# Optimization experiments

Measured on AMD Instinct MI355X. Metric: run time of the kernel, lower is better.

Reference implementation:

```python
import jax, jax.numpy as jnp
import numpy as np

ALPHA = 0.2
TOP_K = 32

def setup_inputs() -> dict:
    key = jax.random.key(0)
    k1, k2, k3, k4, k5 = jax.random.split(key, 5)
    B, T, N, D = 2, 12, 8192, 256
    X = jax.random.normal(k1, (B, T, N, D), dtype=jnp.float32)
    E1 = jax.random.normal(k2, (N, D), dtype=jnp.float32)
    E2 = jax.random.normal(k3, (N, D), dtype=jnp.float32)
    theta1 = jax.random.normal(k4, (D, D), dtype=jnp.float32)
    theta2 = jax.random.normal(k5, (D, D), dtype=jnp.float32)
    a = jnp.float32(1.0)
    return {"X": X, "E1": E1, "E2": E2, "theta1": theta1, "theta2": theta2, "a": a}

def reference(X, E1, E2, theta1, theta2, a):
    # X: [B, T, N, D]
    N = X.shape[2]
    X0 = X.mean(axis=1)[0]  # [N, D], mean over time, first batch element
    # Row-wise L2 normalize (F.normalize with eps=1e-12)
    norm = jnp.maximum(jnp.linalg.norm(X0, axis=1, keepdims=True), 1e-12)
    X_norm = X0 / norm
    sim = X_norm @ X_norm.T  # [N, N] cosine similarity
    sim = sim * (1.0 - jnp.eye(N, dtype=sim.dtype))  # zero diagonal
    topk_vals, topk_idx = jax.lax.top_k(sim, TOP_K)  # [N, K]
    rows = jnp.arange(N)[:, None]
    A_base = jnp.zeros_like(sim).at[rows, topk_idx].set(topk_vals)
    # Adaptive dependency matrix
    M1 = jnp.tanh(ALPHA * (E1 @ theta1))  # [N, D]
    M2 = jnp.tanh(ALPHA * (E2 @ theta2))  # [N, D]
    diff = M1 @ M2.T - M2 @ M1.T  # [N, N], antisymmetric
    adaptive = jax.nn.relu(jnp.tanh(a * diff))
    return adaptive * A_base
```

## Files before the change

kernel.cpp:

```cpp
#include <hip/hip_runtime.h>
#include <hip/hip_bf16.h>
#include <hip/hip_fp16.h>
#include <float.h>
#include <math.h>

#define NN 8192
#define DD 256
#define TT 12
#define TOPK 32
#define NQ 4
#define CAP 56
#define UCAP 64
#define TAU0 0.146875f
#define B2 2.2e-3f
#define DIFFCUT 3.0f

typedef __attribute__((ext_vector_type(8))) _Float16 f16x8;
typedef __attribute__((ext_vector_type(16))) float f32x16;
typedef __attribute__((ext_vector_type(4))) float f32x4;

__device__ __forceinline__ unsigned short f2h(float x) {
    __half h = __float2half(x);
    return *(unsigned short*)&h;
}
__device__ __forceinline__ float h2f(unsigned short v) {
    __half h = *(__half*)&v;
    return __half2float(h);
}

__global__ __launch_bounds__(256) void k_mean_norm(const float* __restrict__ X,
                                                   float* __restrict__ Xn,
                                                   unsigned short* __restrict__ Xpk) {
    const int row = blockIdx.x;
    const int d = threadIdx.x;
    const float* base = X + (size_t)row * DD + d;
    double s = 0.0;
#pragma unroll
    for (int t = 0; t < TT; ++t) s += (double)base[(size_t)t * NN * DD];
    const double mean = s / 12.0;

    double ss = mean * mean;
#pragma unroll
    for (int o = 32; o > 0; o >>= 1) ss += __shfl_down(ss, o, 64);
    __shared__ double wss[4];
    const int lane = threadIdx.x & 63, w = threadIdx.x >> 6;
    if (lane == 0) wss[w] = ss;
    __syncthreads();
    double nrm = sqrt(wss[0] + wss[1] + wss[2] + wss[3]);
    if (nrm < 1e-12) nrm = 1e-12;
    const float xv = (float)(mean / nrm);
    Xn[(size_t)row * DD + d] = xv;

    const int cb = row >> 5;
    const int ks = d >> 4;
    const int l = (row & 31) + 32 * ((d >> 3) & 1);
    const int e = d & 7;
    Xpk[(((size_t)cb * 16 + ks) * 64 + l) * 8 + e] = f2h(xv);
}

__global__ __launch_bounds__(256, 3) void k_simcand_M(
    const unsigned short* __restrict__ Xpk,
    const float* __restrict__ E1, const float* __restrict__ E2,
    const float* __restrict__ th1, const float* __restrict__ th2,
    float* __restrict__ M1, float* __restrict__ M2,
    unsigned int* __restrict__ Mpk,
    unsigned short* __restrict__ cand, float* __restrict__ candv,
    int* __restrict__ counts, float* __restrict__ out) {
    __shared__ __align__(16) unsigned char smem[27264];

    const int tid = threadIdx.x;
    const int g = blockIdx.x;

    if (g < 1280) {
        const int slot = g % 5;
        if (slot == 4) {
            const int zid = g / 5;
            const f32x4 zz = {0.f, 0.f, 0.f, 0.f};
            f32x4* zp = (f32x4*)out + (size_t)zid * 65536 + tid;
#pragma unroll 8
            for (int i = 0; i < 256; ++i)
                __builtin_nontemporal_store(zz, zp + i * 256);
            return;
        }
        unsigned short* a_lds = (unsigned short*)smem;
        int* cnt = (int*)(smem + 16384);
        unsigned short* lst = (unsigned short*)(smem + 16512);
        float* lstv = (float*)(smem + 20096);

        const int simIdx = (g / 5) * 4 + slot;
        const int nt = tid >> 6, lane = tid & 63;
        const int bx = simIdx & 255;
        const int quarter = simIdx >> 8;
        const int r0 = bx * 32;

        {
            const f32x4* src = (const f32x4*)(Xpk + (size_t)bx * 8192);
            f32x4* dst = (f32x4*)a_lds;
            for (int i = tid; i < 1024; i += 256) dst[i] = src[i];
        }
        for (int i = tid; i < 32; i += 256) cnt[i] = 0;
        __syncthreads();

        const int rowL = (lane >> 5) << 2;
        const int colL = lane & 31;
        const unsigned short* arow = a_lds + lane * 8;

        for (int c = 0; c < 16; ++c) {
            const int cbB = quarter * 64 + c * 4 + nt;
            const int gcol = cbB * 32 + colL;
            const size_t bbase = ((size_t)cbB * 16) * 512 + lane * 8;

            f16x8 b[16];
#pragma unroll
            for (int ks = 0; ks < 16; ++ks)
                b[ks] = *(const f16x8*)(Xpk + bbase + ks * 512);

            f32x16 acc;
#pragma unroll
            for (int q = 0; q < 16; ++q) acc[q] = 0.f;
#pragma unroll
            for (int ks = 0; ks < 16; ++ks)
                acc = __builtin_amdgcn_mfma_f32_32x32x16_f16(
                    *(const f16x8*)(arow + ks * 512), b[ks], acc, 0, 0, 0);

#pragma unroll
            for (int reg = 0; reg < 16; ++reg) {
                const float v = acc[reg];
                if (v > TAU0) {
                    const int rl = rowL + (reg & 3) + ((reg >> 2) << 3);
                    if (r0 + rl != gcol) {
                        const int idx = atomicAdd(&cnt[rl], 1);
                        if (idx < CAP) {
                            lst[rl * CAP + idx] = (unsigned short)gcol;
                            lstv[rl * CAP + idx] = v;
                        }
                    }
                }
            }
        }
        __syncthreads();
        for (int i = tid; i < 32; i += 256) {
            int n = cnt[i];
            counts[(r0 + i) * NQ + quarter] = n > CAP ? CAP : n;
        }
        for (int i = tid; i < 32 * CAP; i += 256) {
            const int rl = i / CAP, k = i % CAP;
            int n = cnt[rl];
            if (n > CAP) n = CAP;
            if (k < n) {
                const size_t o = ((size_t)(r0 + rl) * NQ + quarter) * CAP + k;
                cand[o] = lst[rl * CAP + k];
                candv[o] = lstv[rl * CAP + k];
            }
        }
    } else {
        float* e1 = (float*)smem;
        float* e2 = (float*)(smem + 8192);
        const int r0 = (g - 1280) * 8;
        {
            const f32x4* E14 = (const f32x4*)(E1 + (size_t)r0 * DD);
            const f32x4* E24 = (const f32x4*)(E2 + (size_t)r0 * DD);
            f32x4* e14 = (f32x4*)e1;
            f32x4* e24 = (f32x4*)e2;
            for (int i = tid; i < 512; i += 256) {
                e14[i] = E14[i];
                e24[i] = E24[i];
            }
        }
        __syncthreads();
        const int j = tid;
        float a1[8], a2[8];
#pragma unroll
        for (int r = 0; r < 8; ++r) { a1[r] = 0.f; a2[r] = 0.f; }
        for (int k = 0; k < DD; k += 4) {
            float t1[4], t2[4];
#pragma unroll
            for (int kk = 0; kk < 4; ++kk) {
                t1[kk] = th1[(size_t)(k + kk) * DD + j];
                t2[kk] = th2[(size_t)(k + kk) * DD + j];
            }
#pragma unroll
            for (int r = 0; r < 8; ++r) {
                const f32x4 ev1 = *(const f32x4*)&e1[r * DD + k];
                const f32x4 ev2 = *(const f32x4*)&e2[r * DD + k];
                a1[r] += ev1.x * t1[0];
                a1[r] += ev1.y * t1[1];
                a1[r] += ev1.z * t1[2];
                a1[r] += ev1.w * t1[3];
                a2[r] += ev2.x * t2[0];
                a2[r] += ev2.y * t2[1];
                a2[r] += ev2.z * t2[2];
                a2[r] += ev2.w * t2[3];
            }
        }
#pragma unroll
        for (int r = 0; r < 8; ++r) {
            const float m1v = tanhf(0.2f * a1[r]);
            const float m2v = tanhf(0.2f * a2[r]);
            M1[(size_t)(r0 + r) * DD + j] = m1v;
            M2[(size_t)(r0 + r) * DD + j] = m2v;
            Mpk[(size_t)(r0 + r) * DD + j] =
                ((unsigned)f2h(m2v) << 16) | (unsigned)f2h(m1v);
        }
    }
}

__global__ __launch_bounds__(256) void k_refine(
    const float* __restrict__ Xn, const unsigned short* __restrict__ cand,
    const float* __restrict__ candv, const int* __restrict__ counts,
    const float* __restrict__ M1, const float* __restrict__ M2,
    const unsigned int* __restrict__ Mpk, const float* __restrict__ a_ptr,
    float* __restrict__ out) {
    __shared__ float xi[DD], m1i[DD], m2i[DD];
    __shared__ unsigned short cidx[NQ * CAP];
    __shared__ float cs[NQ * CAP];
    __shared__ int carr[NQ], offs[NQ + 1];
    __shared__ unsigned short uidx[UCAP];
    __shared__ float ue[UCAP];
    __shared__ int nUs, ms;
    __shared__ float wv[TOPK];
    __shared__ int wj[TOPK];

    const int i = blockIdx.x, t = threadIdx.x;

    xi[t]  = Xn[(size_t)i * DD + t];
    m1i[t] = M1[(size_t)i * DD + t];
    m2i[t] = M2[(size_t)i * DD + t];
    if (t < NQ) {
        int n = counts[i * NQ + t];
        carr[t] = n < 0 ? 0 : (n > CAP ? CAP : n);
    }
    if (t < TOPK) { wv[t] = 0.f; wj[t] = i; }
    if (t == 0) { nUs = 0; ms = 0; }
    __syncthreads();
    if (t == 0) {
        int s = 0;
#pragma unroll
        for (int q = 0; q < NQ; ++q) { offs[q] = s; s += carr[q]; }
        offs[NQ] = s;
    }
    __syncthreads();
    const int nc = offs[NQ];
#pragma unroll
    for (int q = 0; q < NQ; ++q)
        if (t < carr[q]) {
            const size_t o = ((size_t)i * NQ + q) * CAP + t;
            cidx[offs[q] + t] = cand[o];
            cs[offs[q] + t] = candv[o];
        }
    __syncthreads();

    if (t < nc) {
        const float vc = cs[t];
        int possAbove = 0, certAbove = 0;
        for (int k = 0; k < nc; ++k) {
            const float vk = cs[k];
            possAbove += (vk >= vc - B2);
            certAbove += (vk > vc + B2);
        }
        possAbove -= 1;
        if (possAbove <= TOPK - 1) {
            const int slot = atomicAdd(&ms, 1);
            wv[slot] = vc;
            wj[slot] = cidx[t];
        } else if (certAbove < TOPK) {
            const int p = atomicAdd(&nUs, 1);
            if (p < UCAP) uidx[p] = cidx[t];
        }
    }
    __syncthreads();
    const int m = ms;
    int nU = nUs;
    if (nU > UCAP) nU = UCAP;

    if (nU > 0) {
        const int dl = t & 15, cg = t >> 4;
        for (int base = 0; base < nU; base += 16) {
            const int c = base + cg;
            float p = 0.f;
            if (c < nU) {
                const int j = uidx[c];
                const f32x4* xj4 = (const f32x4*)(Xn + (size_t)j * DD) + dl * 4;
                const f32x4* xi4 = (const f32x4*)xi + dl * 4;
#pragma unroll
                for (int q = 0; q < 4; ++q) {
                    const f32x4 A = xi4[q], B = xj4[q];
                    p += A.x * B.x;
                    p += A.y * B.y;
                    p += A.z * B.z;
                    p += A.w * B.w;
                }
            }
#pragma unroll
            for (int o = 1; o < 16; o <<= 1) p += __shfl_xor(p, o, 64);
            if (c < nU && dl == 0) ue[c] = p;
        }
        __syncthreads();
        if (t < nU && m < TOPK) {
            const float vc = ue[t];
            const int jc = uidx[t];
            int r = 0;
            for (int k = 0; k < nU; ++k) {
                const float vk = ue[k];
                r += (vk > vc) || (vk == vc && uidx[k] < jc);
            }
            if (r < TOPK - m) {
                wv[m + r] = vc;
                wj[m + r] = jc;
            }
        }
        __syncthreads();
    }

    const float a = *a_ptr;
    const int g = t >> 3, lg = t & 7;
    const int j = wj[g];
    const float v = wv[g];

    float p1 = 0.f;
    {
        const uint4* mp = (const uint4*)(Mpk + (size_t)j * DD) + lg * 8;
#pragma unroll
        for (int q = 0; q < 8; ++q) {
            const uint4 u = mp[q];
            const int d = lg * 32 + q * 4;
            p1 += m1i[d + 0] * h2f((unsigned short)(u.x >> 16)) -
                  m2i[d + 0] * h2f((unsigned short)(u.x & 0xffff));
            p1 += m1i[d + 1] * h2f((unsigned short)(u.y >> 16)) -
                  m2i[d + 1] * h2f((unsigned short)(u.y & 0xffff));
            p1 += m1i[d + 2] * h2f((unsigned short)(u.z >> 16)) -
                  m2i[d + 2] * h2f((unsigned short)(u.z & 0xffff));
            p1 += m1i[d + 3] * h2f((unsigned short)(u.w >> 16)) -
                  m2i[d + 3] * h2f((unsigned short)(u.w & 0xffff));
        }
    }
#pragma unroll
    for (int o = 4; o > 0; o >>= 1) p1 += __shfl_xor(p1, o, 64);

    float diff = p1;
    if (fabsf(diff) < DIFFCUT) {
        const f32x4* m1j4 = (const f32x4*)(M1 + (size_t)j * DD) + lg * 8;
        const f32x4* m2j4 = (const f32x4*)(M2 + (size_t)j * DD) + lg * 8;
        float p = 0.f;
        const int dbase = lg * 32;
#pragma unroll
        for (int q = 0; q < 8; ++q) {
            const f32x4 b1 = m1j4[q], b2 = m2j4[q];
            const int d = dbase + q * 4;
            p += m1i[d + 0] * b2.x - m2i[d + 0] * b1.x;
            p += m1i[d + 1] * b2.y - m2i[d + 1] * b1.y;
            p += m1i[d + 2] * b2.z - m2i[d + 2] * b1.z;
            p += m1i[d + 3] * b2.w - m2i[d + 3] * b1.w;
        }
#pragma unroll
        for (int o = 4; o > 0; o >>= 1) p += __shfl_xor(p, o, 64);
        diff = p;
    }
    if (lg == 0 && j != i) {
        float ad = tanhf(a * diff);
        ad = ad > 0.f ? ad : 0.f;
        out[(size_t)i * NN + j] = ad * v;
    }
}

extern "C" void kernel_launch(void* const* d_in, const int* in_sizes, int n_in,
                              void* d_out, int out_size, void* d_ws, size_t ws_size,
                              hipStream_t stream) {
    const float* X   = (const float*)d_in[0];
    const float* E1  = (const float*)d_in[1];
    const float* E2  = (const float*)d_in[2];
    const float* th1 = (const float*)d_in[3];
    const float* th2 = (const float*)d_in[4];
    const float* a   = (const float*)d_in[5];
    float* out = (float*)d_out;

    float* ws = (float*)d_ws;
    float* Xn = ws;
    float* M1 = Xn + (size_t)NN * DD;
    float* M2 = M1 + (size_t)NN * DD;
    unsigned short* Xpk = (unsigned short*)(M2 + (size_t)NN * DD);
    unsigned int* Mpk = (unsigned int*)(Xpk + (size_t)NN * DD);
    unsigned short* cand = (unsigned short*)(Mpk + (size_t)NN * DD);
    float* candv = (float*)(cand + (size_t)NN * NQ * CAP);
    int* counts = (int*)(candv + (size_t)NN * NQ * CAP);

    k_mean_norm<<<NN, 256, 0, stream>>>(X, Xn, Xpk);
    k_simcand_M<<<2304, 256, 0, stream>>>(Xpk, E1, E2, th1, th2,
                                          M1, M2, Mpk,
                                          cand, candv, counts, out);
    k_refine<<<NN, 256, 0, stream>>>(Xn, cand, candv, counts, M1, M2, Mpk, a, out);
}
```

Baseline: 252.4 us.

## Retile similarity GEMM to 64-row blocks with double-buffered LDS staging, move zeroing to refine

The similarity/candidate kernel now computes 64x256 output tiles per block, four waves in a 2x2 arrangement, with 4 accumulators each. A and B fragments are staged into LDS through global_load_lds with double buffering over the K steps, replacing per-wave direct global loads of B. A 32-row A tile is no longer held whole in LDS. The output zeroing blocks are removed from this kernel. Instead each refine block zeroes its own output row before scattering. This cuts redundant global traffic and raises MFMA reuse, at the cost of higher LDS use, lower occupancy (launch bounds 2) and an extra barrier per K step.

```diff
diff --git a/kernel.cpp b/kernel.cpp
--- a/kernel.cpp
+++ b/kernel.cpp
@@ -28,6 +28,12 @@
     return __half2float(h);
 }
 
+__device__ __forceinline__ void glds16(const unsigned short* g, unsigned short* l) {
+    __builtin_amdgcn_global_load_lds(
+        (__attribute__((address_space(1))) const void*)g,
+        (__attribute__((address_space(3))) void*)l, 16, 0, 0);
+}
+
 __global__ __launch_bounds__(256) void k_mean_norm(const float* __restrict__ X,
                                                    float* __restrict__ Xn,
                                                    unsigned short* __restrict__ Xpk) {
@@ -58,7 +64,7 @@
     Xpk[(((size_t)cb * 16 + ks) * 64 + l) * 8 + e] = f2h(xv);
 }
 
-__global__ __launch_bounds__(256, 3) void k_simcand_M(
+__global__ __launch_bounds__(256, 2) void k_simcand_M(
     const unsigned short* __restrict__ Xpk,
     const float* __restrict__ E1, const float* __restrict__ E2,
     const float* __restrict__ th1, const float* __restrict__ th2,
@@ -66,84 +72,96 @@
     unsigned int* __restrict__ Mpk,
     unsigned short* __restrict__ cand, float* __restrict__ candv,
     int* __restrict__ counts, float* __restrict__ out) {
-    __shared__ __align__(16) unsigned char smem[27264];
+    __shared__ __align__(16) unsigned char smem[62720];
 
     const int tid = threadIdx.x;
     const int g = blockIdx.x;
 
-    if (g < 1280) {
-        const int slot = g % 5;
-        if (slot == 4) {
-            const int zid = g / 5;
-            const f32x4 zz = {0.f, 0.f, 0.f, 0.f};
-            f32x4* zp = (f32x4*)out + (size_t)zid * 65536 + tid;
-#pragma unroll 8
-            for (int i = 0; i < 256; ++i)
-                __builtin_nontemporal_store(zz, zp + i * 256);
-            return;
-        }
-        unsigned short* a_lds = (unsigned short*)smem;
-        int* cnt = (int*)(smem + 16384);
-        unsigned short* lst = (unsigned short*)(smem + 16512);
-        float* lstv = (float*)(smem + 20096);
-
-        const int simIdx = (g / 5) * 4 + slot;
-        const int nt = tid >> 6, lane = tid & 63;
-        const int bx = simIdx & 255;
-        const int quarter = simIdx >> 8;
-        const int r0 = bx * 32;
-
-        {
-            const f32x4* src = (const f32x4*)(Xpk + (size_t)bx * 8192);
-            f32x4* dst = (f32x4*)a_lds;
-            for (int i = tid; i < 1024; i += 256) dst[i] = src[i];
-        }
-        for (int i = tid; i < 32; i += 256) cnt[i] = 0;
+    if (g < 512) {
+        int* cnt = (int*)(smem + 40960);
+        unsigned short* lst = (unsigned short*)(smem + 41216);
+        float* lstv = (float*)(smem + 48384);
+
+        const int w = tid >> 6, lane = tid & 63;
+        const int wr = w >> 1, wc = w & 1;
+        const int bx = g & 127;
+        const int quarter = g >> 7;
+        const int r0 = bx * 64;
+
+        auto stage = [&](int uu) {
+            const int s = uu & 7, ct = uu >> 3;
+            unsigned short* dst = (unsigned short*)(smem + (uu & 1) * 20480);
+            {
+                const int i = w >> 1, j = w & 1;
+                glds16(Xpk + (((size_t)(bx * 2 + i) * 16 + (2 * s + j)) << 9) + lane * 8,
+                       dst + w * 512);
+            }
+#pragma unroll
+            for (int q = 0; q < 4; ++q) {
+                const int ch = w * 4 + q, i = ch >> 1, j = ch & 1;
+                glds16(Xpk + (((size_t)(quarter * 64 + ct * 8 + i) * 16 + (2 * s + j)) << 9) + lane * 8,
+                       dst + 2048 + ch * 512);
+            }
+        };
+
+        stage(0);
+        for (int i = tid; i < 64; i += 256) cnt[i] = 0;
         __syncthreads();
 
-        const int rowL = (lane >> 5) << 2;
+        const int rowL = wr * 32 + ((lane >> 5) << 2);
         const int colL = lane & 31;
-        const unsigned short* arow = a_lds + lane * 8;
-
-        for (int c = 0; c < 16; ++c) {
-            const int cbB = quarter * 64 + c * 4 + nt;
-            const int gcol = cbB * 32 + colL;
-            const size_t bbase = ((size_t)cbB * 16) * 512 + lane * 8;
-
-            f16x8 b[16];
-#pragma unroll
-            for (int ks = 0; ks < 16; ++ks)
-                b[ks] = *(const f16x8*)(Xpk + bbase + ks * 512);
-
-            f32x16 acc;
-#pragma unroll
-            for (int q = 0; q < 16; ++q) acc[q] = 0.f;
-#pragma unroll
-            for (int ks = 0; ks < 16; ++ks)
-                acc = __builtin_amdgcn_mfma_f32_32x32x16_f16(
-                    *(const f16x8*)(arow + ks * 512), b[ks], acc, 0, 0, 0);
-
-#pragma unroll
-            for (int reg = 0; reg < 16; ++reg) {
-                const float v = acc[reg];
-                if (v > TAU0) {
-                    const int rl = rowL + (reg & 3) + ((reg >> 2) << 3);
-                    if (r0 + rl != gcol) {
-                        const int idx = atomicAdd(&cnt[rl], 1);
-                        if (idx < CAP) {
-                            lst[rl * CAP + idx] = (unsigned short)gcol;
-                            lstv[rl * CAP + idx] = v;
+
+        for (int ct = 0; ct < 8; ++ct) {
+            f32x16 acc[4];
+#pragma unroll
+            for (int fc = 0; fc < 4; ++fc)
+#pragma unroll
+                for (int q = 0; q < 16; ++q) acc[fc][q] = 0.f;
+
+            for (int s = 0; s < 8; ++s) {
+                const int u = ct * 8 + s;
+                if (u < 63) stage(u + 1);
+
+                const unsigned short* cur = (const unsigned short*)(smem + (u & 1) * 20480);
+                const f16x8 a0 = *(const f16x8*)(cur + (wr * 2 + 0) * 512 + lane * 8);
+                const f16x8 a1 = *(const f16x8*)(cur + (wr * 2 + 1) * 512 + lane * 8);
+#pragma unroll
+                for (int fc = 0; fc < 4; ++fc) {
+                    const int ci = wc * 4 + fc;
+                    const f16x8 b0 = *(const f16x8*)(cur + 2048 + (ci * 2 + 0) * 512 + lane * 8);
+                    const f16x8 b1 = *(const f16x8*)(cur + 2048 + (ci * 2 + 1) * 512 + lane * 8);
+                    acc[fc] = __builtin_amdgcn_mfma_f32_32x32x16_f16(a0, b0, acc[fc], 0, 0, 0);
+                    acc[fc] = __builtin_amdgcn_mfma_f32_32x32x16_f16(a1, b1, acc[fc], 0, 0, 0);
+                }
+                __syncthreads();
+            }
+
+#pragma unroll
+            for (int fc = 0; fc < 4; ++fc) {
+                const int cbB = quarter * 64 + ct * 8 + wc * 4 + fc;
+                const int gcol = cbB * 32 + colL;
+#pragma unroll
+                for (int reg = 0; reg < 16; ++reg) {
+                    const float v = acc[fc][reg];
+                    if (v > TAU0) {
+                        const int rl = rowL + (reg & 3) + ((reg >> 2) << 3);
+                        if (r0 + rl != gcol) {
+                            const int idx = atomicAdd(&cnt[rl], 1);
+                            if (idx < CAP) {
+                                lst[rl * CAP + idx] = (unsigned short)gcol;
+                                lstv[rl * CAP + idx] = v;
+                            }
                         }
                     }
                 }
             }
         }
         __syncthreads();
-        for (int i = tid; i < 32; i += 256) {
+        for (int i = tid; i < 64; i += 256) {
             int n = cnt[i];
             counts[(r0 + i) * NQ + quarter] = n > CAP ? CAP : n;
         }
-        for (int i = tid; i < 32 * CAP; i += 256) {
+        for (int i = tid; i < 64 * CAP; i += 256) {
             const int rl = i / CAP, k = i % CAP;
             int n = cnt[rl];
             if (n > CAP) n = CAP;
@@ -156,7 +174,7 @@
     } else {
         float* e1 = (float*)smem;
         float* e2 = (float*)(smem + 8192);
-        const int r0 = (g - 1280) * 8;
+        const int r0 = (g - 512) * 8;
         {
             const f32x4* E14 = (const f32x4*)(E1 + (size_t)r0 * DD);
             const f32x4* E24 = (const f32x4*)(E2 + (size_t)r0 * DD);
@@ -226,6 +244,13 @@
     xi[t]  = Xn[(size_t)i * DD + t];
     m1i[t] = M1[(size_t)i * DD + t];
     m2i[t] = M2[(size_t)i * DD + t];
+    {
+        const f32x4 zz = {0.f, 0.f, 0.f, 0.f};
+        f32x4* zp = (f32x4*)(out + (size_t)i * NN) + t;
+#pragma unroll
+        for (int q = 0; q < 8; ++q)
+            __builtin_nontemporal_store(zz, zp + q * 256);
+    }
     if (t < NQ) {
         int n = counts[i * NQ + t];
         carr[t] = n < 0 ? 0 : (n > CAP ? CAP : n);
@@ -385,7 +410,7 @@
     int* counts = (int*)(candv + (size_t)NN * NQ * CAP);
 
     k_mean_norm<<<NN, 256, 0, stream>>>(X, Xn, Xpk);
-    k_simcand_M<<<2304, 256, 0, stream>>>(Xpk, E1, E2, th1, th2,
+    k_simcand_M<<<1536, 256, 0, stream>>>(Xpk, E1, E2, th1, th2,
                                           M1, M2, Mpk,
                                           cand, candv, counts, out);
     k_refine<<<NN, 256, 0, stream>>>(Xn, cand, candv, counts, M1, M2, Mpk, a, out);
```

After: 265.3 us. 1.05x slower.
